# Performance work log

Measured on AMD Instinct MI355X. Metric: run time of the kernel, lower is better.

## Reference

```python
import jax, jax.numpy as jnp
import numpy as np

B, D = 4096, 2048


def setup_inputs() -> dict:
    key = jax.random.key(0)
    k1, k2 = jax.random.split(key)
    drug_probs = jax.random.uniform(k1, (B, D), dtype=jnp.float32)
    ddi_matrix = jax.random.normal(k2, (D, D), dtype=jnp.float32)
    return {"drug_probs": drug_probs, "ddi_matrix": ddi_matrix}


def _ddi_upper(ddi_matrix):
    # load_ddi_matrix: binarize, symmetrize via max, zero diagonal; then triu(k=1)
    b = (ddi_matrix > 0).astype(ddi_matrix.dtype)
    b = jnp.maximum(b, b.T)
    d = b.shape[0]
    b = b * (1.0 - jnp.eye(d, dtype=b.dtype))
    upper = jnp.triu(b, k=1)
    normalizer = jnp.maximum(upper.sum(), 1.0)  # clamp(min=1.0)
    return upper, normalizer


def reference(drug_probs, ddi_matrix):
    upper, normalizer = _ddi_upper(ddi_matrix)
    # x^T M x per sample via GEMM + rowwise dot, avoiding the (B,D,D) outer product
    xu = drug_probs @ upper                      # (B, D)
    penalties = jnp.sum(xu * drug_probs, axis=1) / normalizer  # (B,)
    return penalties.mean()  # reduction='mean'
```

## Files before the change

kernel.cpp:

```cpp
#include <hip/hip_runtime.h>
#include <stdint.h>

#define D_DIM 2048
#define B_DIM 4096
#define BMT 128
#define BKB 128
#define NKS (B_DIM / 128)
#define NSPL 6
#define NTILE (D_DIM / BMT)
#define NPAIR ((NTILE * (NTILE + 1)) / 2)
#define GRAM_BLOCKS (NPAIR * NSPL)
#define MWORDS (D_DIM / 64)
#define NT32 (D_DIM / 64)
#define MPAIR ((NT32 * (NT32 + 1)) / 2)
#define TP_BLOCKS ((D_DIM / 64) * (B_DIM / 64))

typedef __attribute__((ext_vector_type(4))) float f32x4;
typedef __attribute__((ext_vector_type(4))) int   i32x4;
typedef __attribute__((ext_vector_type(8))) int   i32x8;

__device__ __forceinline__ void gload16(const void* g, void* lds) {
    __builtin_amdgcn_global_load_lds((__attribute__((address_space(1))) void*)g,
                                     (__attribute__((address_space(3))) void*)lds,
                                     16, 0, 0);
}

__global__ __launch_bounds__(256) void prep_kernel(
    const float* __restrict__ X, const float* __restrict__ ddi,
    unsigned char* __restrict__ XT8, unsigned long long* __restrict__ mask64,
    int* __restrict__ partials, float* __restrict__ gsum)
{
    __shared__ float tile[64][65];
    __shared__ int redi[4];
    const int tid = threadIdx.x;

    if (blockIdx.x < TP_BLOCKS) {
        if (blockIdx.x == 0 && tid == 0) *gsum = 0.f;
        const int i0 = (blockIdx.x & 31) * 64;
        const int k0 = (blockIdx.x >> 5) * 64;

        const int c4 = tid & 15;
        const int rr = tid >> 4;
        #pragma unroll
        for (int p = 0; p < 4; ++p) {
            const int kr = p * 16 + rr;
            const float4 v = *reinterpret_cast<const float4*>(
                &X[(size_t)(k0 + kr) * D_DIM + i0 + c4 * 4]);
            tile[kr][c4 * 4 + 0] = v.x;
            tile[kr][c4 * 4 + 1] = v.y;
            tile[kr][c4 * 4 + 2] = v.z;
            tile[kr][c4 * 4 + 3] = v.w;
        }
        __syncthreads();

        const int ir16 = tid >> 4;
        const int kq   = tid & 15;
        #pragma unroll
        for (int pi = 0; pi < 4; ++pi) {
            const int ir = pi * 16 + ir16;
            const int kc = kq * 4;
            int pk = __builtin_amdgcn_cvt_pk_fp8_f32(tile[kc + 0][ir], tile[kc + 1][ir], 0, false);
            pk     = __builtin_amdgcn_cvt_pk_fp8_f32(tile[kc + 2][ir], tile[kc + 3][ir], pk, true);
            *reinterpret_cast<int*>(XT8 + (size_t)(i0 + ir) * B_DIM + k0 + kc) = pk;
        }
    } else {
        const int mb = blockIdx.x - TP_BLOCKS;
        int bi = 0, rem = mb;
        while (rem >= NT32 - bi) { rem -= NT32 - bi; ++bi; }
        const int bj = bi + rem;
        const int r0 = bi * 64;
        const int c0 = bj * 64;

        const int c4 = tid & 15;
        const int rr = tid >> 4;
        #pragma unroll
        for (int p = 0; p < 4; ++p) {
            const int kr = p * 16 + rr;
            const float4 v = *reinterpret_cast<const float4*>(
                &ddi[(size_t)(c0 + kr) * D_DIM + r0 + c4 * 4]);
            tile[kr][c4 * 4 + 0] = v.x;
            tile[kr][c4 * 4 + 1] = v.y;
            tile[kr][c4 * 4 + 2] = v.z;
            tile[kr][c4 * 4 + 3] = v.w;
        }
        __syncthreads();

        const int lane = tid & 63;
        const int w    = tid >> 6;
        int cnt = 0;
        #pragma unroll
        for (int rr2 = 0; rr2 < 16; ++rr2) {
            const int li = w * 16 + rr2;
            const int gi = r0 + li;
            const int gj = c0 + lane;
            const float a  = ddi[(size_t)gi * D_DIM + c0 + lane];
            const float at = tile[lane][li];
            const bool bit = (gi < gj) && (a > 0.f || at > 0.f);
            const unsigned long long word = __ballot(bit);
            if (lane == 0) mask64[(size_t)gi * MWORDS + bj] = word;
            cnt += bit ? 1 : 0;
        }
        #pragma unroll
        for (int off = 32; off > 0; off >>= 1) cnt += __shfl_down(cnt, off, 64);
        if (lane == 0) redi[w] = cnt;
        __syncthreads();
        if (tid == 0) partials[mb] = redi[0] + redi[1] + redi[2] + redi[3];
    }
}

__device__ __forceinline__ i32x8 frag_read(const unsigned char* ls, int row, int g) {
    const int s = (2 * g) ^ (row & 7);
    const i32x4 lo = *reinterpret_cast<const i32x4*>(ls + row * BKB + s * 16);
    const i32x4 hi = *reinterpret_cast<const i32x4*>(ls + row * BKB + (s ^ 1) * 16);
    i32x8 r;
    r[0] = lo[0]; r[1] = lo[1]; r[2] = lo[2]; r[3] = lo[3];
    r[4] = hi[0]; r[5] = hi[1]; r[6] = hi[2]; r[7] = hi[3];
    return r;
}

__global__ __launch_bounds__(256) void gram_masked_kernel(
    const unsigned char* __restrict__ XT8,
    const unsigned long long* __restrict__ mask64,
    float* __restrict__ gsum)
{
    __shared__ __align__(16) unsigned char lsA[BMT * BKB];
    __shared__ __align__(16) unsigned char lsB[BMT * BKB];
    __shared__ float redf[4];

    const int tid  = threadIdx.x;
    const int lane = tid & 63;
    const int w    = tid >> 6;
    const int wr   = w >> 1, wc = w & 1;
    const int m16  = lane & 15;
    const int g    = lane >> 4;

    const int bid = blockIdx.x;
    const int logical = (bid & 7) * (GRAM_BLOCKS / 8) + (bid >> 3);
    const int pair = logical / NSPL;
    const int s    = logical % NSPL;

    int ti = 0, rem = pair;
    while (rem >= NTILE - ti) { rem -= NTILE - ti; ++ti; }
    const int tj = ti + rem;
    const int i0 = ti * BMT, j0 = tj * BMT;

    const int ks0 = (NKS * s) / NSPL;
    const int ks1 = (NKS * (s + 1)) / NSPL;
    const int nkt = ks1 - ks0;
    const int kbase = ks0 * BKB;

    f32x4 acc[4][4];
    #pragma unroll
    for (int a = 0; a < 4; ++a)
        #pragma unroll
        for (int b = 0; b < 4; ++b)
            acc[a][b] = (f32x4){0.f, 0.f, 0.f, 0.f};

    size_t gaoff[4], gboff[4];
    #pragma unroll
    for (int p = 0; p < 4; ++p) {
        const int chunk = p * 256 + tid;
        const int row = chunk >> 3;
        const int sc = (chunk & 7) ^ (row & 7);
        gaoff[p] = (size_t)(i0 + row) * B_DIM + kbase + sc * 16;
        gboff[p] = (size_t)(j0 + row) * B_DIM + kbase + sc * 16;
    }
    char* lbaseA = (char*)lsA + (size_t)w * 1024;
    char* lbaseB = (char*)lsB + (size_t)w * 1024;

    for (int kt = 0; kt < nkt; ++kt) {
        const int koff = kt * BKB;
        #pragma unroll
        for (int p = 0; p < 4; ++p) {
            gload16(XT8 + gaoff[p] + koff, lbaseA + p * 4096);
            gload16(XT8 + gboff[p] + koff, lbaseB + p * 4096);
        }
        __syncthreads();

        i32x8 aF[4], bF[4];
        #pragma unroll
        for (int f = 0; f < 4; ++f) {
            aF[f] = frag_read(lsA, wr * 64 + f * 16 + m16, g);
            bF[f] = frag_read(lsB, wc * 64 + f * 16 + m16, g);
        }
        #pragma unroll
        for (int fi = 0; fi < 4; ++fi)
            #pragma unroll
            for (int fj = 0; fj < 4; ++fj)
                acc[fi][fj] = __builtin_amdgcn_mfma_scale_f32_16x16x128_f8f6f4(
                    aF[fi], bF[fj], acc[fi][fj],
                    0 , 0 ,
                    0, 0x7F7F7F7F ,
                    0, 0x7F7F7F7F );

        __syncthreads();
    }

    float lsum = 0.f;
    const int jb = (j0 + wc * 64) >> 6;
    #pragma unroll
    for (int fi = 0; fi < 4; ++fi) {
        #pragma unroll
        for (int r = 0; r < 4; ++r) {
            const int i = i0 + wr * 64 + fi * 16 + g * 4 + r;
            unsigned long long wword = 0ull;
            if (jb * 64 + 63 > i) wword = mask64[(size_t)i * MWORDS + jb];
            #pragma unroll
            for (int fj = 0; fj < 4; ++fj) {
                if ((wword >> (fj * 16 + m16)) & 1ull) lsum += acc[fi][fj][r];
            }
        }
    }
    #pragma unroll
    for (int off = 32; off > 0; off >>= 1) lsum += __shfl_down(lsum, off, 64);
    if (lane == 0) redf[w] = lsum;
    __syncthreads();
    if (tid == 0) atomicAdd(gsum, redf[0] + redf[1] + redf[2] + redf[3]);
}

__global__ __launch_bounds__(256) void finalize_kernel(
    const float* __restrict__ gsum, const int* __restrict__ partials,
    float* __restrict__ out)
{
    __shared__ int redi[4];
    const int tid = threadIdx.x;
    int s = 0;
    for (int i = tid; i < MPAIR; i += 256) s += partials[i];
    #pragma unroll
    for (int off = 32; off > 0; off >>= 1) s += __shfl_down(s, off, 64);
    const int lane = tid & 63, w = tid >> 6;
    if (lane == 0) redi[w] = s;
    __syncthreads();
    if (tid == 0) {
        const int cnt = redi[0] + redi[1] + redi[2] + redi[3];
        out[0] = gsum[0] / ((float)B_DIM * fmaxf((float)cnt, 1.0f));
    }
}

extern "C" void kernel_launch(void* const* d_in, const int* in_sizes, int n_in,
                              void* d_out, int out_size, void* d_ws, size_t ws_size,
                              hipStream_t stream) {
    const float* X   = (const float*)d_in[0];
    const float* ddi = (const float*)d_in[1];
    float* out = (float*)d_out;

    const size_t XT_BYTES   = (size_t)D_DIM * B_DIM;
    const size_t MASK_BYTES = (size_t)D_DIM * MWORDS * sizeof(unsigned long long);
    const size_t PART_BYTES = (size_t)MPAIR * sizeof(int);
    if (ws_size < XT_BYTES + MASK_BYTES + PART_BYTES + 16) return;

    unsigned char* XT8 = (unsigned char*)d_ws;
    unsigned long long* mask64 = (unsigned long long*)((char*)d_ws + XT_BYTES);
    int*   partials = (int*)((char*)d_ws + XT_BYTES + MASK_BYTES);
    float* gsum     = (float*)((char*)d_ws + XT_BYTES + MASK_BYTES + PART_BYTES);

    prep_kernel<<<TP_BLOCKS + MPAIR, 256, 0, stream>>>(X, ddi, XT8, mask64, partials, gsum);
    gram_masked_kernel<<<GRAM_BLOCKS, 256, 0, stream>>>(XT8, mask64, gsum);
    finalize_kernel<<<1, 256, 0, stream>>>(gsum, partials, out);
}
```

Before: 44.32 us.

## Double-buffer gram tiles, rebalance split-K, fuse finalize via last-block ticket

Double-buffers the LDS tiles in the masked gram kernel so the next k-slice's global-to-LDS loads are issued before the current slice's MFMAs, and drops one barrier per iteration. Replaces the uniform 6-way split-K with 4-way splits for the first 104 tile pairs and 3-way for the rest, giving fewer, larger blocks. Removes the finalize kernel: the pair count is accumulated atomically in prep, and the last gram block, found with a ticket counter, writes the output. A memset now initializes the counters. This doubles LDS per block, which may lower occupancy, and adds atomic contention on the shared counter.

```diff
diff --git a/kernel.cpp b/kernel.cpp
--- a/kernel.cpp
+++ b/kernel.cpp
@@ -6,10 +6,10 @@
 #define BMT 128
 #define BKB 128
 #define NKS (B_DIM / 128)
-#define NSPL 6
 #define NTILE (D_DIM / BMT)
 #define NPAIR ((NTILE * (NTILE + 1)) / 2)
-#define GRAM_BLOCKS (NPAIR * NSPL)
+#define P4 104
+#define GRAM_BLOCKS (P4 * 4 + (NPAIR - P4) * 3)
 #define MWORDS (D_DIM / 64)
 #define NT32 (D_DIM / 64)
 #define MPAIR ((NT32 * (NT32 + 1)) / 2)
@@ -28,14 +28,13 @@
 __global__ __launch_bounds__(256) void prep_kernel(
     const float* __restrict__ X, const float* __restrict__ ddi,
     unsigned char* __restrict__ XT8, unsigned long long* __restrict__ mask64,
-    int* __restrict__ partials, float* __restrict__ gsum)
+    int* __restrict__ gcnt)
 {
     __shared__ float tile[64][65];
     __shared__ int redi[4];
     const int tid = threadIdx.x;
 
     if (blockIdx.x < TP_BLOCKS) {
-        if (blockIdx.x == 0 && tid == 0) *gsum = 0.f;
         const int i0 = (blockIdx.x & 31) * 64;
         const int k0 = (blockIdx.x >> 5) * 64;
 
@@ -104,7 +103,7 @@
         for (int off = 32; off > 0; off >>= 1) cnt += __shfl_down(cnt, off, 64);
         if (lane == 0) redi[w] = cnt;
         __syncthreads();
-        if (tid == 0) partials[mb] = redi[0] + redi[1] + redi[2] + redi[3];
+        if (tid == 0) atomicAdd(gcnt, redi[0] + redi[1] + redi[2] + redi[3]);
     }
 }
 
@@ -121,11 +120,13 @@
 __global__ __launch_bounds__(256) void gram_masked_kernel(
     const unsigned char* __restrict__ XT8,
     const unsigned long long* __restrict__ mask64,
-    float* __restrict__ gsum)
+    float* __restrict__ gsum, int* __restrict__ gcnt, int* __restrict__ ticket,
+    float* __restrict__ out)
 {
-    __shared__ __align__(16) unsigned char lsA[BMT * BKB];
-    __shared__ __align__(16) unsigned char lsB[BMT * BKB];
+    __shared__ __align__(16) unsigned char lsA[2][BMT * BKB];
+    __shared__ __align__(16) unsigned char lsB[2][BMT * BKB];
     __shared__ float redf[4];
+    __shared__ int lastFlag;
 
     const int tid  = threadIdx.x;
     const int lane = tid & 63;
@@ -136,16 +137,18 @@
 
     const int bid = blockIdx.x;
     const int logical = (bid & 7) * (GRAM_BLOCKS / 8) + (bid >> 3);
-    const int pair = logical / NSPL;
-    const int s    = logical % NSPL;
+
+    int pair, s, ns;
+    if (logical < P4 * 4) { pair = logical >> 2; s = logical & 3; ns = 4; }
+    else { const int t = logical - P4 * 4; pair = P4 + t / 3; s = t % 3; ns = 3; }
 
     int ti = 0, rem = pair;
     while (rem >= NTILE - ti) { rem -= NTILE - ti; ++ti; }
     const int tj = ti + rem;
     const int i0 = ti * BMT, j0 = tj * BMT;
 
-    const int ks0 = (NKS * s) / NSPL;
-    const int ks1 = (NKS * (s + 1)) / NSPL;
+    const int ks0 = (NKS * s) / ns;
+    const int ks1 = (NKS * (s + 1)) / ns;
     const int nkt = ks1 - ks0;
     const int kbase = ks0 * BKB;
 
@@ -165,23 +168,29 @@
         gaoff[p] = (size_t)(i0 + row) * B_DIM + kbase + sc * 16;
         gboff[p] = (size_t)(j0 + row) * B_DIM + kbase + sc * 16;
     }
-    char* lbaseA = (char*)lsA + (size_t)w * 1024;
-    char* lbaseB = (char*)lsB + (size_t)w * 1024;
-
+
+    auto stage = [&](int buf, int kt) {
+        char* bA = (char*)lsA[buf] + (size_t)w * 1024;
+        char* bB = (char*)lsB[buf] + (size_t)w * 1024;
+        const int koff = kt * BKB;
+        #pragma unroll
+        for (int p = 0; p < 4; ++p) {
+            gload16(XT8 + gaoff[p] + koff, bA + p * 4096);
+            gload16(XT8 + gboff[p] + koff, bB + p * 4096);
+        }
+    };
+
+    stage(0, 0);
+    __syncthreads();
+    int cur = 0;
     for (int kt = 0; kt < nkt; ++kt) {
-        const int koff = kt * BKB;
-        #pragma unroll
-        for (int p = 0; p < 4; ++p) {
-            gload16(XT8 + gaoff[p] + koff, lbaseA + p * 4096);
-            gload16(XT8 + gboff[p] + koff, lbaseB + p * 4096);
-        }
-        __syncthreads();
+        if (kt + 1 < nkt) stage(cur ^ 1, kt + 1);
 
         i32x8 aF[4], bF[4];
         #pragma unroll
         for (int f = 0; f < 4; ++f) {
-            aF[f] = frag_read(lsA, wr * 64 + f * 16 + m16, g);
-            bF[f] = frag_read(lsB, wc * 64 + f * 16 + m16, g);
+            aF[f] = frag_read(lsA[cur], wr * 64 + f * 16 + m16, g);
+            bF[f] = frag_read(lsB[cur], wc * 64 + f * 16 + m16, g);
         }
         #pragma unroll
         for (int fi = 0; fi < 4; ++fi)
@@ -193,7 +202,10 @@
                     0, 0x7F7F7F7F ,
                     0, 0x7F7F7F7F );
 
-        __syncthreads();
+        if (kt + 1 < nkt) {
+            __syncthreads();
+            cur ^= 1;
+        }
     }
 
     float lsum = 0.f;
@@ -215,25 +227,19 @@
     for (int off = 32; off > 0; off >>= 1) lsum += __shfl_down(lsum, off, 64);
     if (lane == 0) redf[w] = lsum;
     __syncthreads();
-    if (tid == 0) atomicAdd(gsum, redf[0] + redf[1] + redf[2] + redf[3]);
-}
-
-__global__ __launch_bounds__(256) void finalize_kernel(
-    const float* __restrict__ gsum, const int* __restrict__ partials,
-    float* __restrict__ out)
-{
-    __shared__ int redi[4];
-    const int tid = threadIdx.x;
-    int s = 0;
-    for (int i = tid; i < MPAIR; i += 256) s += partials[i];
-    #pragma unroll
-    for (int off = 32; off > 0; off >>= 1) s += __shfl_down(s, off, 64);
-    const int lane = tid & 63, w = tid >> 6;
-    if (lane == 0) redi[w] = s;
+
+    if (tid == 0) {
+        atomicAdd(gsum, redf[0] + redf[1] + redf[2] + redf[3]);
+        __threadfence();
+        const int old = atomicAdd(ticket, 1);
+        lastFlag = (old == GRAM_BLOCKS - 1);
+    }
     __syncthreads();
-    if (tid == 0) {
-        const int cnt = redi[0] + redi[1] + redi[2] + redi[3];
-        out[0] = gsum[0] / ((float)B_DIM * fmaxf((float)cnt, 1.0f));
+    if (lastFlag && tid == 0) {
+        __threadfence();
+        const float s2  = atomicAdd(gsum, 0.0f);
+        const int   cnt = atomicAdd(gcnt, 0);
+        out[0] = s2 / ((float)B_DIM * fmaxf((float)cnt, 1.0f));
     }
 }
 
@@ -246,15 +252,16 @@
 
     const size_t XT_BYTES   = (size_t)D_DIM * B_DIM;
     const size_t MASK_BYTES = (size_t)D_DIM * MWORDS * sizeof(unsigned long long);
-    const size_t PART_BYTES = (size_t)MPAIR * sizeof(int);
-    if (ws_size < XT_BYTES + MASK_BYTES + PART_BYTES + 16) return;
+    if (ws_size < XT_BYTES + MASK_BYTES + 64) return;
 
     unsigned char* XT8 = (unsigned char*)d_ws;
     unsigned long long* mask64 = (unsigned long long*)((char*)d_ws + XT_BYTES);
-    int*   partials = (int*)((char*)d_ws + XT_BYTES + MASK_BYTES);
-    float* gsum     = (float*)((char*)d_ws + XT_BYTES + MASK_BYTES + PART_BYTES);
-
-    prep_kernel<<<TP_BLOCKS + MPAIR, 256, 0, stream>>>(X, ddi, XT8, mask64, partials, gsum);
-    gram_masked_kernel<<<GRAM_BLOCKS, 256, 0, stream>>>(XT8, mask64, gsum);
-    finalize_kernel<<<1, 256, 0, stream>>>(gsum, partials, out);
-}
+    char* ctrl = (char*)d_ws + XT_BYTES + MASK_BYTES;
+    float* gsum   = (float*)(ctrl + 0);
+    int*   gcnt   = (int*)(ctrl + 4);
+    int*   ticket = (int*)(ctrl + 8);
+
+    hipMemsetAsync(ctrl, 0, 16, stream);
+    prep_kernel<<<TP_BLOCKS + MPAIR, 256, 0, stream>>>(X, ddi, XT8, mask64, gcnt);
+    gram_masked_kernel<<<GRAM_BLOCKS, 256, 0, stream>>>(XT8, mask64, gsum, gcnt, ticket, out);
+}
```

After: 59.47 us. 34.2% more time.

## Quantize drug probabilities to FP4 and run Gram MFMA in fp4 format

Applied to the files above, without the earlier changes.

The prep kernel now quantizes X (scaled by 4) to 4-bit E2M1 codes using threshold rounding and packs eight values per 32-bit word, halving the transposed buffer size. The Gram kernel reads half-width rows and issues the scaled MFMA in fp4 mode with a block scale that undoes the factor of 4, doing two 128-wide K steps per loaded tile. This halves memory traffic and LDS footprint per K element and uses the faster fp4 MFMA rate. The cost is much coarser quantization of uniform [0,1) inputs, which may exceed the accuracy tolerance.

```diff
diff --git a/kernel.cpp b/kernel.cpp
--- a/kernel.cpp
+++ b/kernel.cpp
@@ -5,7 +5,8 @@
 #define B_DIM 4096
 #define BMT 128
 #define BKB 128
-#define NKS (B_DIM / 128)
+#define ROWB (B_DIM / 2)
+#define NKS4 (B_DIM / 256)
 #define NSPL 6
 #define NTILE (D_DIM / BMT)
 #define NPAIR ((NTILE * (NTILE + 1)) / 2)
@@ -27,7 +28,7 @@
 
 __global__ __launch_bounds__(256) void prep_kernel(
     const float* __restrict__ X, const float* __restrict__ ddi,
-    unsigned char* __restrict__ XT8, unsigned long long* __restrict__ mask64,
+    unsigned char* __restrict__ XT4, unsigned long long* __restrict__ mask64,
     int* __restrict__ partials, float* __restrict__ gsum)
 {
     __shared__ float tile[64][65];
@@ -53,15 +54,22 @@
         }
         __syncthreads();
 
-        const int ir16 = tid >> 4;
-        const int kq   = tid & 15;
-        #pragma unroll
-        for (int pi = 0; pi < 4; ++pi) {
-            const int ir = pi * 16 + ir16;
-            const int kc = kq * 4;
-            int pk = __builtin_amdgcn_cvt_pk_fp8_f32(tile[kc + 0][ir], tile[kc + 1][ir], 0, false);
-            pk     = __builtin_amdgcn_cvt_pk_fp8_f32(tile[kc + 2][ir], tile[kc + 3][ir], pk, true);
-            *reinterpret_cast<int*>(XT8 + (size_t)(i0 + ir) * B_DIM + k0 + kc) = pk;
+        const int kq8 = tid & 7;
+        const int irr = tid >> 3;
+        #pragma unroll
+        for (int p = 0; p < 2; ++p) {
+            const int ir = p * 32 + irr;
+            unsigned int pk = 0;
+            #pragma unroll
+            for (int e = 0; e < 8; ++e) {
+                const float y = 4.0f * tile[kq8 * 8 + e][ir];
+                const unsigned int c = (unsigned)(y >= 0.25f) + (unsigned)(y >= 0.75f)
+                                     + (unsigned)(y >= 1.25f) + (unsigned)(y >= 1.75f)
+                                     + (unsigned)(y >= 2.5f)  + (unsigned)(y >= 3.5f);
+                pk |= c << (4 * e);
+            }
+            *reinterpret_cast<unsigned int*>(
+                XT4 + (size_t)(i0 + ir) * ROWB + (k0 >> 1) + kq8 * 4) = pk;
         }
     } else {
         const int mb = blockIdx.x - TP_BLOCKS;
@@ -108,18 +116,15 @@
     }
 }
 
-__device__ __forceinline__ i32x8 frag_read(const unsigned char* ls, int row, int g) {
-    const int s = (2 * g) ^ (row & 7);
+__device__ __forceinline__ i32x8 frag_read4(const unsigned char* ls, int row, int g, int c) {
+    const int s = (4 * c + g) ^ (row & 7);
     const i32x4 lo = *reinterpret_cast<const i32x4*>(ls + row * BKB + s * 16);
-    const i32x4 hi = *reinterpret_cast<const i32x4*>(ls + row * BKB + (s ^ 1) * 16);
-    i32x8 r;
-    r[0] = lo[0]; r[1] = lo[1]; r[2] = lo[2]; r[3] = lo[3];
-    r[4] = hi[0]; r[5] = hi[1]; r[6] = hi[2]; r[7] = hi[3];
+    i32x8 r = {lo[0], lo[1], lo[2], lo[3], 0, 0, 0, 0};
     return r;
 }
 
 __global__ __launch_bounds__(256) void gram_masked_kernel(
-    const unsigned char* __restrict__ XT8,
+    const unsigned char* __restrict__ XT4,
     const unsigned long long* __restrict__ mask64,
     float* __restrict__ gsum)
 {
@@ -144,8 +149,8 @@
     const int tj = ti + rem;
     const int i0 = ti * BMT, j0 = tj * BMT;
 
-    const int ks0 = (NKS * s) / NSPL;
-    const int ks1 = (NKS * (s + 1)) / NSPL;
+    const int ks0 = (NKS4 * s) / NSPL;
+    const int ks1 = (NKS4 * (s + 1)) / NSPL;
     const int nkt = ks1 - ks0;
     const int kbase = ks0 * BKB;
 
@@ -162,8 +167,8 @@
         const int chunk = p * 256 + tid;
         const int row = chunk >> 3;
         const int sc = (chunk & 7) ^ (row & 7);
-        gaoff[p] = (size_t)(i0 + row) * B_DIM + kbase + sc * 16;
-        gboff[p] = (size_t)(j0 + row) * B_DIM + kbase + sc * 16;
+        gaoff[p] = (size_t)(i0 + row) * ROWB + kbase + sc * 16;
+        gboff[p] = (size_t)(j0 + row) * ROWB + kbase + sc * 16;
     }
     char* lbaseA = (char*)lsA + (size_t)w * 1024;
     char* lbaseB = (char*)lsB + (size_t)w * 1024;
@@ -172,26 +177,29 @@
         const int koff = kt * BKB;
         #pragma unroll
         for (int p = 0; p < 4; ++p) {
-            gload16(XT8 + gaoff[p] + koff, lbaseA + p * 4096);
-            gload16(XT8 + gboff[p] + koff, lbaseB + p * 4096);
-        }
-        __syncthreads();
-
-        i32x8 aF[4], bF[4];
-        #pragma unroll
-        for (int f = 0; f < 4; ++f) {
-            aF[f] = frag_read(lsA, wr * 64 + f * 16 + m16, g);
-            bF[f] = frag_read(lsB, wc * 64 + f * 16 + m16, g);
-        }
-        #pragma unroll
-        for (int fi = 0; fi < 4; ++fi)
-            #pragma unroll
-            for (int fj = 0; fj < 4; ++fj)
-                acc[fi][fj] = __builtin_amdgcn_mfma_scale_f32_16x16x128_f8f6f4(
-                    aF[fi], bF[fj], acc[fi][fj],
-                    0 , 0 ,
-                    0, 0x7F7F7F7F ,
-                    0, 0x7F7F7F7F );
+            gload16(XT4 + gaoff[p] + koff, lbaseA + p * 4096);
+            gload16(XT4 + gboff[p] + koff, lbaseB + p * 4096);
+        }
+        __syncthreads();
+
+        #pragma unroll
+        for (int c = 0; c < 2; ++c) {
+            i32x8 aF[4], bF[4];
+            #pragma unroll
+            for (int f = 0; f < 4; ++f) {
+                aF[f] = frag_read4(lsA, wr * 64 + f * 16 + m16, g, c);
+                bF[f] = frag_read4(lsB, wc * 64 + f * 16 + m16, g, c);
+            }
+            #pragma unroll
+            for (int fi = 0; fi < 4; ++fi)
+                #pragma unroll
+                for (int fj = 0; fj < 4; ++fj)
+                    acc[fi][fj] = __builtin_amdgcn_mfma_scale_f32_16x16x128_f8f6f4(
+                        aF[fi], bF[fj], acc[fi][fj],
+                        4 , 4 ,
+                        0, 0x7D7D7D7D ,
+                        0, 0x7D7D7D7D );
+        }
 
         __syncthreads();
     }
@@ -244,17 +252,17 @@
     const float* ddi = (const float*)d_in[1];
     float* out = (float*)d_out;
 
-    const size_t XT_BYTES   = (size_t)D_DIM * B_DIM;
+    const size_t XT_BYTES   = (size_t)D_DIM * ROWB;
     const size_t MASK_BYTES = (size_t)D_DIM * MWORDS * sizeof(unsigned long long);
     const size_t PART_BYTES = (size_t)MPAIR * sizeof(int);
-    if (ws_size < XT_BYTES + MASK_BYTES + PART_BYTES + 16) return;
-
-    unsigned char* XT8 = (unsigned char*)d_ws;
+    if (ws_size < XT_BYTES + MASK_BYTES + PART_BYTES + 64) return;
+
+    unsigned char* XT4 = (unsigned char*)d_ws;
     unsigned long long* mask64 = (unsigned long long*)((char*)d_ws + XT_BYTES);
     int*   partials = (int*)((char*)d_ws + XT_BYTES + MASK_BYTES);
     float* gsum     = (float*)((char*)d_ws + XT_BYTES + MASK_BYTES + PART_BYTES);
 
-    prep_kernel<<<TP_BLOCKS + MPAIR, 256, 0, stream>>>(X, ddi, XT8, mask64, partials, gsum);
-    gram_masked_kernel<<<GRAM_BLOCKS, 256, 0, stream>>>(XT8, mask64, gsum);
+    prep_kernel<<<TP_BLOCKS + MPAIR, 256, 0, stream>>>(X, ddi, XT4, mask64, partials, gsum);
+    gram_masked_kernel<<<GRAM_BLOCKS, 256, 0, stream>>>(XT4, mask64, gsum);
     finalize_kernel<<<1, 256, 0, stream>>>(gsum, partials, out);
 }
```

Result: faster. 38.84 us (-12.4%).
